# Kernel optimization log

Measured on AMD Instinct MI355X. Metric: run time of the kernel, lower is better.

## Reference

```python
import jax, jax.numpy as jnp
import numpy as np

N_PRED = 10000
N_GT = 1000
NUM_CLASSES = 80
IMG_H = 800
IMG_W = 1333
EPS = 1e-12
ALPHA, GAMMA, CLS_W = 0.25, 2.0, 2.0
L1_W, IOU_W = 5.0, 2.0
CENTER_RADIUS = 2.5
CAND_TOPK = 5


def _make_boxes(key, n, w, h):
    k1, k2 = jax.random.split(key)
    cxcy = jax.random.uniform(k1, (n, 2)) * jnp.array([w, h], jnp.float32)
    wh = jax.random.uniform(k2, (n, 2)) * 190.0 + 10.0
    return jnp.concatenate([cxcy - wh / 2, cxcy + wh / 2], axis=1).astype(jnp.float32)


def setup_inputs() -> dict:
    key = jax.random.key(0)
    k1, k2, k3, k4 = jax.random.split(key, 4)
    return {
        'pred_logits': jax.random.normal(k1, (N_PRED, NUM_CLASSES), jnp.float32),
        'pred_boxes': _make_boxes(k2, N_PRED, IMG_W, IMG_H),
        'gt_bboxes': _make_boxes(k3, N_GT, IMG_W, IMG_H),
        'gt_labels': jax.random.randint(k4, (N_GT,), 0, NUM_CLASSES),
        'img_h': IMG_H,
        'img_w': IMG_W,
    }


def _pairwise_iou_giou(pred, gt):
    area_p = (pred[:, 2] - pred[:, 0]) * (pred[:, 3] - pred[:, 1])
    area_g = (gt[:, 2] - gt[:, 0]) * (gt[:, 3] - gt[:, 1])
    lt = jnp.maximum(pred[:, None, :2], gt[None, :, :2])
    rb = jnp.minimum(pred[:, None, 2:], gt[None, :, 2:])
    wh = jnp.clip(rb - lt, 0.0)
    inter = wh[..., 0] * wh[..., 1]                       # [N,G]
    union = area_p[:, None] + area_g[None, :] - inter
    iou = inter / jnp.maximum(union, EPS)
    elt = jnp.minimum(pred[:, None, :2], gt[None, :, :2])
    erb = jnp.maximum(pred[:, None, 2:], gt[None, :, 2:])
    ewh = jnp.clip(erb - elt, 0.0)
    enclose = ewh[..., 0] * ewh[..., 1]
    giou = iou - (enclose - union) / jnp.maximum(enclose, EPS)
    return iou, giou


def _center_info(pred, gt):
    # pred/gt in xyxy; uses pred box centers, strict inequalities as in source
    pcx = (pred[:, 0] + pred[:, 2]) * 0.5
    pcy = (pred[:, 1] + pred[:, 3]) * 0.5
    gx1, gy1, gx2, gy2 = gt[:, 0], gt[:, 1], gt[:, 2], gt[:, 3]
    in_boxes = ((pcx[:, None] > gx1) & (pcx[:, None] < gx2) &
                (pcy[:, None] > gy1) & (pcy[:, None] < gy2))
    gcx, gcy = (gx1 + gx2) * 0.5, (gy1 + gy2) * 0.5
    gw, gh = gx2 - gx1, gy2 - gy1
    r = CENTER_RADIUS
    in_centers = ((pcx[:, None] > gcx - r * gw) & (pcx[:, None] < gcx + r * gw) &
                  (pcy[:, None] > gcy - r * gh) & (pcy[:, None] < gcy + r * gh))
    valid = in_boxes.any(1) | in_centers.any(1)
    return valid, in_boxes & in_centers


def _compute_cost_and_ious(pred_logits, pred_boxes, gt_bboxes, gt_labels, img_h, img_w):
    # FocalLossCost
    p = jax.nn.sigmoid(pred_logits)
    neg = -jnp.log1p(-(p - EPS)) * (1 - ALPHA) * p ** GAMMA
    pos = -jnp.log(p + EPS) * ALPHA * (1 - p) ** GAMMA
    cls_cost = (pos - neg)[:, gt_labels] * CLS_W            # [N,G]
    # BBoxL1Cost (normalized by image size)
    factor = jnp.array([img_w, img_h, img_w, img_h], jnp.float32)
    l1_cost = jnp.sum(jnp.abs(pred_boxes[:, None, :] / factor -
                              gt_bboxes[None, :, :] / factor), -1) * L1_W
    # IoUCost (giou) + pairwise ious for dynamic-k
    ious, giou = _pairwise_iou_giou(pred_boxes, gt_bboxes)
    iou_cost = -giou * IOU_W
    valid_mask, in_boxes_and_center = _center_info(pred_boxes, gt_bboxes)
    cost = cls_cost + l1_cost + iou_cost + jnp.where(in_boxes_and_center, 0.0, 100.0)
    cost = cost + jnp.where(valid_mask, 0.0, 10000.0)[:, None]
    return cost, ious


def _dynamic_k_matching(cost, ious):
    n, g = cost.shape
    k = min(CAND_TOPK, n)
    topk_ious, _ = jax.lax.top_k(ious.T, k)                 # [G,k]
    dynamic_ks = jnp.maximum(topk_ious.sum(1).astype(jnp.int32), 1)
    _, idx = jax.lax.top_k(-cost.T, k)                      # [G,k] smallest costs per gt
    vals = (jnp.arange(k)[None, :] < dynamic_ks[:, None]).astype(cost.dtype)
    cols = jnp.broadcast_to(jnp.arange(g)[:, None], (g, k))
    mm = jnp.zeros_like(cost).at[idx, cols].max(vals)       # scatter 1s per gt column
    # resolve priors matched to >1 gt (note: mask is reused stale inside the loop, as in source)
    prior_mask = mm.sum(1) > 1
    cmin = jnp.argmin(cost, axis=1)
    mm = jnp.where(prior_mask[:, None], jax.nn.one_hot(cmin, g, dtype=cost.dtype), mm)

    def cond(state):
        m, _ = state
        return jnp.any(m.sum(0) == 0)

    def body(state):
        m, c = state
        matched_q = m.sum(1) > 0
        c = c + 100000.0 * matched_q[:, None].astype(c.dtype)
        unmatched = m.sum(0) == 0
        pos = jnp.argmin(c, axis=0)                         # [G]
        oh = jax.nn.one_hot(pos, n, dtype=c.dtype).T        # [N,G]
        m = jnp.where(unmatched[None, :], oh, m)
        cmin2 = jnp.argmin(c, axis=1)
        m_fix = jnp.where(prior_mask[:, None], jax.nn.one_hot(cmin2, g, dtype=c.dtype), m)
        m = jnp.where(jnp.any(m.sum(1) > 1), m_fix, m)
        return (m, c)

    mm, _ = jax.lax.while_loop(cond, body, (mm, cost))
    fg_mask = mm.sum(1) > 0
    matched = jnp.argmax(mm, axis=1).astype(jnp.int32)
    return fg_mask, jnp.where(fg_mask, matched, 0)


def reference(pred_logits, pred_boxes, gt_bboxes, gt_labels, img_h, img_w):
    cost, ious = _compute_cost_and_ious(pred_logits, pred_boxes, gt_bboxes,
                                        gt_labels, img_h, img_w)
    fg_mask, matched_gt = _dynamic_k_matching(cost, ious)
    # dense form: matched_gt[i] valid only where fg_mask[i] (fixed-shape version of
    # the original's compressed matched_gt_inds = mm[fg_mask].argmax(1))
    return fg_mask, matched_gt
```

## Files before the change

### kernel.cpp

```cpp
#include <hip/hip_runtime.h>
#include <cfloat>
#include <cmath>

#define NP 10000
#define NG 1000
#define NC 80
#define LMAX 6
#define NCH 4
#define CHSZ (NP / NCH)
#define WMAIN 39
#define WTAIL 4

#define S_MULTI 12
#define S_BODY  16
#define RI_BIG  0x3fffffff
#define KMAX    0xFFFFFFFFFFFFFFFFull

#define TKEY    0xC248000000000000ull

#define WCAP    768

__device__ __forceinline__ bool lexless(float av, int ai, float bv, int bi) {
    return (av < bv) || (av == bv && ai < bi);
}

__device__ __forceinline__ unsigned long long packkey(float v, int idx) {
    unsigned u = __float_as_uint(v);
    u ^= (unsigned)(((int)u) >> 31) | 0x80000000u;
    return ((unsigned long long)u << 32) | (unsigned)idx;
}
__device__ __forceinline__ int keyidx(unsigned long long k) {
    return (int)(unsigned)(k & 0xFFFFFFFFu);
}

__device__ __forceinline__ float inflate(float c, int k) {
    for (int q = 0; q < k; q++) c += 100000.0f;
    return c;
}

__device__ __forceinline__ void cost_iou(float4 p, float4 pn, float4 pi,
        float4 g, float4 cb, float4 Gn, float ga, float clsv,
        float& cc_out, float& iou_out) {
#pragma clang fp contract(off)
    float wx = fminf(p.z, g.z) - fmaxf(p.x, g.x); wx = fmaxf(wx, 0.0f);
    float wy = fminf(p.w, g.w) - fmaxf(p.y, g.y); wy = fmaxf(wy, 0.0f);
    float inter = wx * wy;
    float uni = pi.z + ga - inter;
    float iou = inter / fmaxf(uni, 1e-12f);
    float ex = fmaxf(p.z, g.z) - fminf(p.x, g.x); ex = fmaxf(ex, 0.0f);
    float ey = fmaxf(p.w, g.w) - fminf(p.y, g.y); ey = fmaxf(ey, 0.0f);
    float enc = ex * ey;
    float giou = iou - (enc - uni) / fmaxf(enc, 1e-12f);
    float l1 = ((fabsf(pn.x - Gn.x) + fabsf(pn.y - Gn.y))
                + fabsf(pn.z - Gn.z)) + fabsf(pn.w - Gn.w);
    float cc = clsv + l1 * 5.0f;
    cc = cc + (-giou * 2.0f);
    bool inb = (pi.x > g.x && pi.x < g.z && pi.y > g.y && pi.y < g.w);
    bool inc = (pi.x > cb.x && pi.x < cb.z && pi.y > cb.y && pi.y < cb.w);
    cc = cc + ((inb && inc) ? 0.0f : 100.0f);
    cc = cc + pi.w;
    cc_out = cc; iou_out = iou;
}

__device__ __forceinline__ void ins5k(unsigned long long* kv,
        unsigned long long key) {
    if (key < kv[4]) {
        kv[4] = key;
#pragma unroll
        for (int t = 4; t > 0; t--)
            if (kv[t] < kv[t-1]) { unsigned long long tv = kv[t]; kv[t] = kv[t-1]; kv[t-1] = tv; }
    }
}
__device__ __forceinline__ void ins5i(float* iv, float iou) {
    if (iou > iv[4]) {
        iv[4] = iou;
#pragma unroll
        for (int t = 4; t > 0; t--)
            if (iv[t] > iv[t-1]) { float tv = iv[t]; iv[t] = iv[t-1]; iv[t-1] = tv; }
    }
}

__device__ __forceinline__ void cswapk(unsigned long long& a,
        unsigned long long& b) {
    unsigned long long lo = (a < b) ? a : b;
    unsigned long long hi = (a < b) ? b : a;
    a = lo; b = hi;
}
__device__ __forceinline__ void sort5k(unsigned long long* a) {
    cswapk(a[0],a[1]); cswapk(a[3],a[4]); cswapk(a[2],a[4]);
    cswapk(a[2],a[3]); cswapk(a[1],a[4]); cswapk(a[0],a[3]);
    cswapk(a[0],a[2]); cswapk(a[1],a[3]); cswapk(a[1],a[2]);
}
__device__ __forceinline__ void cswapi(float& a, float& b) {
    float hi = fmaxf(a, b), lo = fminf(a, b);
    a = hi; b = lo;
}
__device__ __forceinline__ void sort5i(float* a) {
    cswapi(a[0],a[1]); cswapi(a[3],a[4]); cswapi(a[2],a[4]);
    cswapi(a[2],a[3]); cswapi(a[1],a[4]); cswapi(a[0],a[3]);
    cswapi(a[0],a[2]); cswapi(a[1],a[3]); cswapi(a[1],a[2]);
}

__device__ __forceinline__ void wavemerge5(unsigned long long* kv, float* iv) {
#pragma unroll
    for (int d = 1; d < 64; d <<= 1) {
        unsigned long long r0 = __shfl_xor(kv[0], d);
        unsigned long long r1 = __shfl_xor(kv[1], d);
        unsigned long long r2 = __shfl_xor(kv[2], d);
        unsigned long long r3 = __shfl_xor(kv[3], d);
        unsigned long long r4 = __shfl_xor(kv[4], d);
        kv[0] = (kv[0] < r4) ? kv[0] : r4;
        kv[1] = (kv[1] < r3) ? kv[1] : r3;
        kv[2] = (kv[2] < r2) ? kv[2] : r2;
        kv[3] = (kv[3] < r1) ? kv[3] : r1;
        kv[4] = (kv[4] < r0) ? kv[4] : r0;
        sort5k(kv);
        float s0 = __shfl_xor(iv[0], d);
        float s1 = __shfl_xor(iv[1], d);
        float s2 = __shfl_xor(iv[2], d);
        float s3 = __shfl_xor(iv[3], d);
        float s4 = __shfl_xor(iv[4], d);
        iv[0] = fmaxf(iv[0], s4);
        iv[1] = fmaxf(iv[1], s3);
        iv[2] = fmaxf(iv[2], s2);
        iv[3] = fmaxf(iv[3], s1);
        iv[4] = fmaxf(iv[4], s0);
        sort5i(iv);
    }
}

#define CLS_TI 64
#define PB_CLS0 40
#define PB_G0   197
#define PB_V0   201
__global__ __launch_bounds__(256) void k_prep(const float* __restrict__ logits,
        const float* __restrict__ pb, const float* __restrict__ gb,
        const int* __restrict__ imgw, const int* __restrict__ imgh,
        float* __restrict__ clsval, float4* __restrict__ pnorm,
        float4* __restrict__ pinfo, float4* __restrict__ gcb,
        float4* __restrict__ gnm, float* __restrict__ gar,
        int* rowcnt, int* rowfirst, int* rowiter, int* prior, int* priorcol,
        int* colsum, int* scal)
{
    __shared__ float sl[CLS_TI * (NC + 1)];
    int b = blockIdx.x;
    if (b < PB_CLS0) {
        int i = b * 256 + threadIdx.x;
        if (i < NP) {
            rowcnt[i] = 0; rowfirst[i] = 0x7fffffff; rowiter[i] = RI_BIG;
            prior[i] = 0; priorcol[i] = 0;
        }
        if (i < NG) colsum[i] = 0;
        if (i < 32) scal[i] = 0;
    } else if (b < PB_G0) {
        int i0 = (b - PB_CLS0) * CLS_TI;
        bool full = (i0 + CLS_TI) <= NP;
        if (full) {
            const float* src = logits + (size_t)i0 * NC;
            for (int e = threadIdx.x; e < CLS_TI * NC; e += 256) {
                int di = e / NC, c = e - di * NC;
                sl[di * (NC + 1) + c] = src[e];
            }
        } else {
            for (int e = threadIdx.x; e < CLS_TI * NC; e += 256) {
                int di = e / NC, c = e - di * NC;
                int i = i0 + di;
                sl[di * (NC + 1) + c] = (i < NP) ? logits[(size_t)i * NC + c] : 0.0f;
            }
        }
        __syncthreads();
        for (int e = threadIdx.x; e < CLS_TI * NC; e += 256) {
            int c = e >> 6, di = e & 63;
            int i = i0 + di;
            if (i >= NP) continue;
            float x = sl[di * (NC + 1) + c];
            float p = 1.0f / (1.0f + expf(-x));
            float neg = -log1pf(-(p - 1e-12f)) * 0.75f * (p * p);
            float om = 1.0f - p;
            float pos = -logf(p + 1e-12f) * 0.25f * (om * om);
            clsval[(size_t)c * NP + i] = (pos - neg) * 2.0f;
        }
    } else if (b < PB_V0) {
#pragma clang fp contract(off)
        int j = (b - PB_G0) * 256 + threadIdx.x;
        if (j < NG) {
            float fw = (float)imgw[0], fh = (float)imgh[0];
            float4 g = ((const float4*)gb)[j];
            float gcx = (g.x + g.z) * 0.5f, gcy = (g.y + g.w) * 0.5f;
            float gw = g.z - g.x, gh = g.w - g.y;
            float4 cb; cb.x = gcx - 2.5f * gw; cb.y = gcy - 2.5f * gh;
            cb.z = gcx + 2.5f * gw; cb.w = gcy + 2.5f * gh;
            gcb[j] = cb;
            float4 Gn; Gn.x = g.x / fw; Gn.y = g.y / fh; Gn.z = g.z / fw; Gn.w = g.w / fh;
            gnm[j] = Gn;
            gar[j] = (g.z - g.x) * (g.w - g.y);
        }
    } else {
#pragma clang fp contract(off)
        int wave = threadIdx.x >> 6;
        int lane = threadIdx.x & 63;
        int i = (b - PB_V0) * 4 + wave;
        if (i >= NP) return;
        float4 p = ((const float4*)pb)[i];
        float pcx = (p.x + p.z) * 0.5f, pcy = (p.y + p.w) * 0.5f;
        int vb = 0, vc = 0;
        const float4* gb4 = (const float4*)gb;
        for (int jb = 0; jb < NG; jb += 64) {
            int j = jb + lane;
            if (j < NG) {
                float4 g = gb4[j];
                vb |= (pcx > g.x && pcx < g.z && pcy > g.y && pcy < g.w) ? 1 : 0;
                float gcx = (g.x + g.z) * 0.5f, gcy = (g.y + g.w) * 0.5f;
                float gw = g.z - g.x, gh = g.w - g.y;
                vc |= (pcx > gcx - 2.5f * gw && pcx < gcx + 2.5f * gw &&
                       pcy > gcy - 2.5f * gh && pcy < gcy + 2.5f * gh) ? 1 : 0;
            }
            if (__any(vb | vc)) break;
        }
        int any = __any(vb | vc) ? 1 : 0;
        if (lane == 0) {
            float fw = (float)imgw[0], fh = (float)imgh[0];
            float4 pn; pn.x = p.x / fw; pn.y = p.y / fh; pn.z = p.z / fw; pn.w = p.w / fh;
            pnorm[i] = pn;
            float4 pi4; pi4.x = pcx; pi4.y = pcy;
            pi4.z = (p.z - p.x) * (p.w - p.y);
            pi4.w = any ? 0.0f : 10000.0f;
            pinfo[i] = pi4;
        }
    }
}

__global__ __launch_bounds__(256) void k_cost2(
        const float* __restrict__ pb, const float* __restrict__ gb,
        const int* __restrict__ glab, const float* __restrict__ clsval,
        const float4* __restrict__ pnorm, const float4* __restrict__ pinfo,
        const float4* __restrict__ gcb, const float4* __restrict__ gnm,
        const float* __restrict__ gar,
        int* __restrict__ rowcnt, int* __restrict__ rowfirst,
        int* __restrict__ rowiter, int* __restrict__ top5,
        int* __restrict__ dkarr)
{
    __shared__ int s_list[4 * WCAP];
    __shared__ unsigned long long s_k4[4][5];
    __shared__ float s_iv4[4][5];
    __shared__ int s_redo;

    int j = blockIdx.x;
    int tid = threadIdx.x;
    int wid = tid >> 6;
    int ln  = tid & 63;
    float4 g  = ((const float4*)gb)[j];
    float4 cb = gcb[j];
    float4 Gn = gnm[j];
    float  ga = gar[j];
    const float* clscol = clsval + (size_t)glab[j] * NP;
    const float4* pb4 = (const float4*)pb;
    int base_i = wid * CHSZ;

    int wbase = 0;
    for (int k = 0; k <= WMAIN; k++) {
        bool valid = (k < WMAIN) | (ln < WTAIL);
        int i = base_i + ln + k * 64;
        float4 p = pb4[valid ? i : base_i];
        bool o = valid & (p.z > g.x) & (g.z > p.x) & (p.w > g.y) & (g.w > p.y);
        unsigned long long m = __ballot(o ? 1 : 0);
        if (o) {
            int slot = wbase + __popcll(m & ((1ull << ln) - 1ull));
            if (slot < WCAP) s_list[wid * WCAP + slot] = i;
        }
        wbase += __popcll(m);
    }
    int cnt = wbase;
    bool overflow = (cnt > WCAP);

    unsigned long long kv[5]; float iv[5];
#pragma unroll
    for (int t = 0; t < 5; t++) { kv[t] = KMAX; iv[t] = overflow ? -1.0f : 0.0f; }

    if (!overflow) {
        for (int q = ln; q < cnt; q += 64) {
            int i = s_list[wid * WCAP + q];
            float cc, iou;
            cost_iou(pb4[i], pnorm[i], pinfo[i], g, cb, Gn, ga, clscol[i], cc, iou);
            ins5k(kv, packkey(cc, i)); ins5i(iv, iou);
        }
    } else {
        for (int k = 0; k <= WMAIN; k++) {
            bool valid = (k < WMAIN) | (ln < WTAIL);
            if (valid) {
                int i = base_i + ln + k * 64;
                float cc, iou;
                cost_iou(pb4[i], pnorm[i], pinfo[i], g, cb, Gn, ga, clscol[i], cc, iou);
                ins5k(kv, packkey(cc, i)); ins5i(iv, iou);
            }
        }
    }
    wavemerge5(kv, iv);

    if (ln == 0) {
#pragma unroll
        for (int t = 0; t < 5; t++) { s_k4[wid][t] = kv[t]; s_iv4[wid][t] = iv[t]; }
    }
    __syncthreads();

    unsigned long long mk0=KMAX, mk1=KMAX, mk2=KMAX, mk3=KMAX, mk4=KMAX;
    float mi0=-2.0f, mi1=-2.0f, mi2=-2.0f, mi3=-2.0f, mi4=-2.0f;
    if (tid == 0) {
        int h0 = 0, h1 = 0, h2 = 0, h3 = 0;
        unsigned long long mk[5];
#pragma unroll
        for (int r = 0; r < 5; r++) {
            unsigned long long v0 = (h0 < 5) ? s_k4[0][h0] : KMAX;
            unsigned long long v1 = (h1 < 5) ? s_k4[1][h1] : KMAX;
            unsigned long long v2 = (h2 < 5) ? s_k4[2][h2] : KMAX;
            unsigned long long v3 = (h3 < 5) ? s_k4[3][h3] : KMAX;
            unsigned long long best = v0; int sel = 0;
            if (v1 < best) { best = v1; sel = 1; }
            if (v2 < best) { best = v2; sel = 2; }
            if (v3 < best) { best = v3; sel = 3; }
            mk[r] = best;
            h0 += (sel == 0); h1 += (sel == 1); h2 += (sel == 2); h3 += (sel == 3);
        }
        int g0 = 0, g1 = 0, g2 = 0, g3 = 0;
        float mi[5];
#pragma unroll
        for (int r = 0; r < 5; r++) {
            float w0 = (g0 < 5) ? s_iv4[0][g0] : -2.0f;
            float w1 = (g1 < 5) ? s_iv4[1][g1] : -2.0f;
            float w2 = (g2 < 5) ? s_iv4[2][g2] : -2.0f;
            float w3 = (g3 < 5) ? s_iv4[3][g3] : -2.0f;
            float best = w0; int sel = 0;
            if (w1 > best) { best = w1; sel = 1; }
            if (w2 > best) { best = w2; sel = 2; }
            if (w3 > best) { best = w3; sel = 3; }
            mi[r] = best;
            g0 += (sel == 0); g1 += (sel == 1); g2 += (sel == 2); g3 += (sel == 3);
        }
        mk0 = mk[0]; mk1 = mk[1]; mk2 = mk[2]; mk3 = mk[3]; mk4 = mk[4];
        mi0 = mi[0]; mi1 = mi[1]; mi2 = mi[2]; mi3 = mi[3]; mi4 = mi[4];
        s_redo = (mk4 >= TKEY) ? 1 : 0;
    }
    __syncthreads();

    if (s_redo) {
#pragma unroll
        for (int t = 0; t < 5; t++) { kv[t] = KMAX; iv[t] = -1.0f; }
        for (int k = 0; k <= WMAIN; k++) {
            bool valid = (k < WMAIN) | (ln < WTAIL);
            if (valid) {
                int i = base_i + ln + k * 64;
                float cc, iou;
                cost_iou(pb4[i], pnorm[i], pinfo[i], g, cb, Gn, ga, clscol[i], cc, iou);
                ins5k(kv, packkey(cc, i)); ins5i(iv, iou);
            }
        }
        wavemerge5(kv, iv);
        if (ln == 0) {
#pragma unroll
            for (int t = 0; t < 5; t++) { s_k4[wid][t] = kv[t]; s_iv4[wid][t] = iv[t]; }
        }
        __syncthreads();
        if (tid == 0) {
            int h0 = 0, h1 = 0, h2 = 0, h3 = 0;
            unsigned long long mk[5];
#pragma unroll
            for (int r = 0; r < 5; r++) {
                unsigned long long v0 = (h0 < 5) ? s_k4[0][h0] : KMAX;
                unsigned long long v1 = (h1 < 5) ? s_k4[1][h1] : KMAX;
                unsigned long long v2 = (h2 < 5) ? s_k4[2][h2] : KMAX;
                unsigned long long v3 = (h3 < 5) ? s_k4[3][h3] : KMAX;
                unsigned long long best = v0; int sel = 0;
                if (v1 < best) { best = v1; sel = 1; }
                if (v2 < best) { best = v2; sel = 2; }
                if (v3 < best) { best = v3; sel = 3; }
                mk[r] = best;
                h0 += (sel == 0); h1 += (sel == 1); h2 += (sel == 2); h3 += (sel == 3);
            }
            int g0 = 0, g1 = 0, g2 = 0, g3 = 0;
            float mi[5];
#pragma unroll
            for (int r = 0; r < 5; r++) {
                float w0 = (g0 < 5) ? s_iv4[0][g0] : -2.0f;
                float w1 = (g1 < 5) ? s_iv4[1][g1] : -2.0f;
                float w2 = (g2 < 5) ? s_iv4[2][g2] : -2.0f;
                float w3 = (g3 < 5) ? s_iv4[3][g3] : -2.0f;
                float best = w0; int sel = 0;
                if (w1 > best) { best = w1; sel = 1; }
                if (w2 > best) { best = w2; sel = 2; }
                if (w3 > best) { best = w3; sel = 3; }
                mi[r] = best;
                g0 += (sel == 0); g1 += (sel == 1); g2 += (sel == 2); g3 += (sel == 3);
            }
            mk0 = mk[0]; mk1 = mk[1]; mk2 = mk[2]; mk3 = mk[3]; mk4 = mk[4];
            mi0 = mi[0]; mi1 = mi[1]; mi2 = mi[2]; mi3 = mi[3]; mi4 = mi[4];
        }
    }

    if (tid == 0) {
        float s = (((mi0 + mi1) + mi2) + mi3) + mi4;
        int dk = (int)s;
        if (dk < 1) dk = 1;
        dkarr[j] = dk;
        int b0 = keyidx(mk0), b1 = keyidx(mk1), b2 = keyidx(mk2);
        int b3 = keyidx(mk3), b4 = keyidx(mk4);
        top5[j * 5 + 0] = b0; top5[j * 5 + 1] = b1; top5[j * 5 + 2] = b2;
        top5[j * 5 + 3] = b3; top5[j * 5 + 4] = b4;
        int bs0 = b0, bs1 = b1, bs2 = b2, bs3 = b3, bs4 = b4;
#pragma unroll
        for (int t = 0; t < 5; t++) {
            int r = (t == 0) ? bs0 : (t == 1) ? bs1 : (t == 2) ? bs2
                  : (t == 3) ? bs3 : bs4;
            if (t < dk) {
                atomicAdd(&rowcnt[r], 1);
                atomicMin(&rowfirst[r], j);
                atomicMin(&rowiter[r], -1);
            }
        }
    }
}

__global__ __launch_bounds__(256) void k_pfixsurv(const float* __restrict__ pb,
        const float* __restrict__ gb, const int* __restrict__ glab,
        const float* __restrict__ clsval,
        const float4* __restrict__ pnorm, const float4* __restrict__ pinfo,
        const float4* __restrict__ gcb, const float4* __restrict__ gnm,
        const float* __restrict__ gar,
        int* __restrict__ prior, int* __restrict__ priorcol,
        int* __restrict__ colsum,
        const int* __restrict__ rowcnt, const int* __restrict__ top5,
        const int* __restrict__ dkarr)
{
    int b = blockIdx.x;
    int tid = threadIdx.x;
    if (b >= 2500) {
        int j = (b - 2500) * 256 + tid;
        if (j >= NG) return;
        int c = 0;
        int dk = dkarr[j];
        for (int t = 0; t < dk; t++) if (rowcnt[top5[j * 5 + t]] == 1) c++;
        if (c) atomicAdd(&colsum[j], c);
        return;
    }
    __shared__ float rv[256]; __shared__ int ri[256];
    for (int q = 0; q < 4; q++) {
        int row = b * 4 + q;
        if (rowcnt[row] <= 1) continue;
        if (tid == 0) prior[row] = 1;
        float4 p = ((const float4*)pb)[row];
        float4 pn = pnorm[row];
        float4 pi4 = pinfo[row];
        float best = FLT_MAX; int bj = 0x7fffffff;
        for (int j = tid; j < NG; j += 256) {
            float cc, iou;
            cost_iou(p, pn, pi4, ((const float4*)gb)[j], gcb[j], gnm[j], gar[j],
                     clsval[(size_t)glab[j] * NP + row], cc, iou);
            if (lexless(cc, j, best, bj)) { best = cc; bj = j; }
        }
        rv[tid] = best; ri[tid] = bj; __syncthreads();
        for (int w = 128; w > 0; w >>= 1) {
            if (tid < w) {
                float ov = rv[tid + w]; int oi = ri[tid + w];
                if (lexless(ov, oi, rv[tid], ri[tid])) { rv[tid] = ov; ri[tid] = oi; }
            }
            __syncthreads();
        }
        if (tid == 0) {
            priorcol[row] = ri[0];
            atomicAdd(&colsum[ri[0]], 1);
        }
        __syncthreads();
    }
}

__global__ __launch_bounds__(256) void k_iterB(const float* __restrict__ pb,
        const float* __restrict__ gb, const int* __restrict__ glab,
        const float* __restrict__ clsval,
        const float4* __restrict__ pnorm, const float4* __restrict__ pinfo,
        const float4* __restrict__ gcb, const float4* __restrict__ gnm,
        const float* __restrict__ gar, const int* __restrict__ top5,
        int* __restrict__ rowiter, int* __restrict__ rowcnt,
        int* __restrict__ rowfirst, int* __restrict__ colsum,
        int* __restrict__ scal, int t)
{
    int j = blockIdx.x;
    if (colsum[j] != 0) return;
    int tid = threadIdx.x;
    if (tid == 0) scal[S_BODY + t] = 1;

    __shared__ int s_pos;
    if (tid == 0) {
        int pos = -1;
        for (int r = 0; r < 5; r++) {
            int i = top5[j * 5 + r];
            if (rowiter[i] >= t) { pos = i; break; }
        }
        s_pos = pos;
    }
    __syncthreads();
    int pos = s_pos;

    if (pos < 0) {
        float4 g  = ((const float4*)gb)[j];
        float4 cb = gcb[j];
        float4 Gn = gnm[j];
        float  ga = gar[j];
        const float* clscol = clsval + (size_t)glab[j] * NP;
        const float4* pb4 = (const float4*)pb;
        __shared__ float rv[256]; __shared__ int ri[256];
        float best = FLT_MAX; int bi = 0x7fffffff;
        for (int i = tid; i < NP; i += 256) {
            if (rowiter[i] < t) continue;
            float cc, iou;
            cost_iou(pb4[i], pnorm[i], pinfo[i], g, cb, Gn, ga, clscol[i], cc, iou);
            if (lexless(cc, i, best, bi)) { best = cc; bi = i; }
        }
        rv[tid] = best; ri[tid] = bi; __syncthreads();
        for (int w = 128; w > 0; w >>= 1) {
            if (tid < w) {
                float ov = rv[tid + w]; int oi = ri[tid + w];
                if (lexless(ov, oi, rv[tid], ri[tid])) { rv[tid] = ov; ri[tid] = oi; }
            }
            __syncthreads();
        }
        pos = ri[0];
    }

    if (tid == 0) {
        colsum[j] = 1;
        int old = atomicAdd(&rowcnt[pos], 1);
        if (old >= 1) scal[S_MULTI] = 1;
        atomicMin(&rowfirst[pos], j);
        atomicMin(&rowiter[pos], t);
    }
}

__global__ __launch_bounds__(256) void k_iterC(const float* __restrict__ pb,
        const float* __restrict__ gb, const int* __restrict__ glab,
        const float* __restrict__ clsval,
        const float4* __restrict__ pnorm, const float4* __restrict__ pinfo,
        const float4* __restrict__ gcb, const float4* __restrict__ gnm,
        const float* __restrict__ gar,
        const int* __restrict__ prior, const int* __restrict__ rowiter,
        int* __restrict__ priorcol, int* __restrict__ colsum,
        int* __restrict__ scal, int t)
{
    if (scal[S_BODY + t] == 0 || scal[S_MULTI] == 0) return;
    int b = blockIdx.x;
    int tid = threadIdx.x;
    __shared__ float rv[256]; __shared__ int ri[256];
    for (int q = 0; q < 4; q++) {
        int row = b * 4 + q;
        if (!prior[row]) continue;
        int k = t - rowiter[row]; if (k < 0) k = 0;
        float4 p = ((const float4*)pb)[row];
        float4 pn = pnorm[row];
        float4 pi4 = pinfo[row];
        float best = FLT_MAX; int bj = 0x7fffffff;
        for (int j = tid; j < NG; j += 256) {
            float cc, iou;
            cost_iou(p, pn, pi4, ((const float4*)gb)[j], gcb[j], gnm[j], gar[j],
                     clsval[(size_t)glab[j] * NP + row], cc, iou);
            float val = inflate(cc, k);
            if (lexless(val, j, best, bj)) { best = val; bj = j; }
        }
        rv[tid] = best; ri[tid] = bj; __syncthreads();
        for (int w = 128; w > 0; w >>= 1) {
            if (tid < w) {
                float ov = rv[tid + w]; int oi = ri[tid + w];
                if (lexless(ov, oi, rv[tid], ri[tid])) { rv[tid] = ov; ri[tid] = oi; }
            }
            __syncthreads();
        }
        if (tid == 0) {
            int nb = ri[0];
            int oldc = priorcol[row];
            if (nb != oldc) {
                atomicSub(&colsum[oldc], 1);
                atomicAdd(&colsum[nb], 1);
                priorcol[row] = nb;
            }
        }
        __syncthreads();
    }
}

__global__ __launch_bounds__(256) void k_final(const int* __restrict__ rowcnt,
        const int* __restrict__ prior, const int* __restrict__ priorcol,
        const int* __restrict__ rowfirst, int* __restrict__ out)
{
    int i = blockIdx.x * 256 + threadIdx.x;
    if (i >= NP) return;
    int fg = rowcnt[i] > 0;
    out[i] = fg ? 1 : 0;
    out[NP + i] = fg ? (prior[i] ? priorcol[i] : rowfirst[i]) : 0;
}

extern "C" void kernel_launch(void* const* d_in, const int* in_sizes, int n_in,
                              void* d_out, int out_size, void* d_ws, size_t ws_size,
                              hipStream_t stream)
{
    (void)in_sizes; (void)n_in; (void)out_size; (void)ws_size;
    const float* logits = (const float*)d_in[0];
    const float* pboxes = (const float*)d_in[1];
    const float* gboxes = (const float*)d_in[2];
    const int*   glab   = (const int*)d_in[3];
    const int*   imgh   = (const int*)d_in[4];
    const int*   imgw   = (const int*)d_in[5];
    int* out = (int*)d_out;

    char* w = (char*)d_ws;
    float*  clsval  = (float*)(w);
    float4* pnorm   = (float4*)(w + 3200000);
    float4* pinfo   = (float4*)(w + 3360000);
    float4* gcb     = (float4*)(w + 3520000);
    float4* gnm     = (float4*)(w + 3536000);
    float*  gar     = (float*)(w + 3552000);
    int* rowcnt     = (int*)(w + 3556000);
    int* rowfirst   = (int*)(w + 3596000);
    int* rowiter    = (int*)(w + 3636000);
    int* prior      = (int*)(w + 3676000);
    int* priorcol   = (int*)(w + 3716000);
    int* top5       = (int*)(w + 3756000);
    int* dkarr      = (int*)(w + 3776000);
    int* colsum     = (int*)(w + 3780000);
    int* scal       = (int*)(w + 3784000);

    hipLaunchKernelGGL(k_prep, dim3(2701), dim3(256), 0, stream,
                       logits, pboxes, gboxes, imgw, imgh,
                       clsval, pnorm, pinfo, gcb, gnm, gar,
                       rowcnt, rowfirst, rowiter, prior, priorcol, colsum, scal);
    hipLaunchKernelGGL(k_cost2, dim3(NG), dim3(256), 0, stream,
                       pboxes, gboxes, glab, clsval, pnorm, pinfo, gcb, gnm, gar,
                       rowcnt, rowfirst, rowiter, top5, dkarr);
    hipLaunchKernelGGL(k_pfixsurv, dim3(2504), dim3(256), 0, stream,
                       pboxes, gboxes, glab, clsval, pnorm, pinfo, gcb, gnm, gar,
                       prior, priorcol, colsum, rowcnt, top5, dkarr);
    for (int t = 0; t < LMAX; t++) {
        hipLaunchKernelGGL(k_iterB, dim3(NG), dim3(256), 0, stream,
                           pboxes, gboxes, glab, clsval, pnorm, pinfo, gcb, gnm, gar,
                           top5, rowiter, rowcnt, rowfirst, colsum, scal, t);
        hipLaunchKernelGGL(k_iterC, dim3(2500), dim3(256), 0, stream,
                           pboxes, gboxes, glab, clsval, pnorm, pinfo, gcb, gnm, gar,
                           prior, rowiter, priorcol, colsum, scal, t);
    }
    hipLaunchKernelGGL(k_final, dim3(40), dim3(256), 0, stream,
                       rowcnt, prior, priorcol, rowfirst, out);
}
```

Before: 155.0 us.

## Fuse iterative matching loop into single-block persistent kernel with cached prior-row costs

Replaces the 12 per-iteration launches of k_iterB/k_iterC plus k_final with one single-block 1024-thread kernel that runs all iterations internally, using shared-memory lists of prior rows and of columns needing a full scan. k_pfixsurv now caches the cost rows of multi-matched priors in a workspace buffer, so later iterations re-read costs instead of recomputing them. Wave-level shuffle reductions replace the shared-memory tree reductions. This removes launch overhead and redundant cost evaluation, but the whole dynamic phase runs on a single CU, so any fallback full scans over 10000 predictions become much slower.

```diff
diff --git a/kernel.cpp b/kernel.cpp
--- a/kernel.cpp
+++ b/kernel.cpp
@@ -11,14 +11,16 @@
 #define WMAIN 39
 #define WTAIL 4
 
-#define S_MULTI 12
-#define S_BODY  16
 #define RI_BIG  0x3fffffff
 #define KMAX    0xFFFFFFFFFFFFFFFFull
 
 #define TKEY    0xC248000000000000ull
 
 #define WCAP    768
+
+#define PSLOTS  2560
+#define PCAP    2560
+#define FCAP    1024
 
 __device__ __forceinline__ bool lexless(float av, int ai, float bv, int bi) {
     return (av < bv) || (av == bv && ai < bi);
@@ -129,6 +131,15 @@
     }
 }
 
+__device__ __forceinline__ void wavered_lex(float& best, int& bi) {
+#pragma unroll
+    for (int d = 1; d < 64; d <<= 1) {
+        float ov = __shfl_xor(best, d);
+        int oi = __shfl_xor(bi, d);
+        if (lexless(ov, oi, best, bi)) { best = ov; bi = oi; }
+    }
+}
+
 #define CLS_TI 64
 #define PB_CLS0 40
 #define PB_G0   197
@@ -140,7 +151,7 @@
         float4* __restrict__ pinfo, float4* __restrict__ gcb,
         float4* __restrict__ gnm, float* __restrict__ gar,
         int* rowcnt, int* rowfirst, int* rowiter, int* prior, int* priorcol,
-        int* colsum, int* scal)
+        int* colsum, int* scal, int* priorslot)
 {
     __shared__ float sl[CLS_TI * (NC + 1)];
     int b = blockIdx.x;
@@ -148,7 +159,7 @@
         int i = b * 256 + threadIdx.x;
         if (i < NP) {
             rowcnt[i] = 0; rowfirst[i] = 0x7fffffff; rowiter[i] = RI_BIG;
-            prior[i] = 0; priorcol[i] = 0;
+            prior[i] = 0; priorcol[i] = 0; priorslot[i] = -1;
         }
         if (i < NG) colsum[i] = 0;
         if (i < 32) scal[i] = 0;
@@ -405,11 +416,10 @@
         int b3 = keyidx(mk3), b4 = keyidx(mk4);
         top5[j * 5 + 0] = b0; top5[j * 5 + 1] = b1; top5[j * 5 + 2] = b2;
         top5[j * 5 + 3] = b3; top5[j * 5 + 4] = b4;
-        int bs0 = b0, bs1 = b1, bs2 = b2, bs3 = b3, bs4 = b4;
 #pragma unroll
         for (int t = 0; t < 5; t++) {
-            int r = (t == 0) ? bs0 : (t == 1) ? bs1 : (t == 2) ? bs2
-                  : (t == 3) ? bs3 : bs4;
+            int r = (t == 0) ? b0 : (t == 1) ? b1 : (t == 2) ? b2
+                  : (t == 3) ? b3 : b4;
             if (t < dk) {
                 atomicAdd(&rowcnt[r], 1);
                 atomicMin(&rowfirst[r], j);
@@ -428,7 +438,9 @@
         int* __restrict__ prior, int* __restrict__ priorcol,
         int* __restrict__ colsum,
         const int* __restrict__ rowcnt, const int* __restrict__ top5,
-        const int* __restrict__ dkarr)
+        const int* __restrict__ dkarr,
+        int* __restrict__ scal, int* __restrict__ priorslot,
+        float* __restrict__ rowcost)
 {
     int b = blockIdx.x;
     int tid = threadIdx.x;
@@ -442,10 +454,20 @@
         return;
     }
     __shared__ float rv[256]; __shared__ int ri[256];
+    __shared__ int s_slot;
     for (int q = 0; q < 4; q++) {
         int row = b * 4 + q;
         if (rowcnt[row] <= 1) continue;
-        if (tid == 0) prior[row] = 1;
+        if (tid == 0) {
+            prior[row] = 1;
+            int s = atomicAdd(&scal[20], 1);
+            int sl = (s < PSLOTS) ? s : -1;
+            priorslot[row] = sl;
+            s_slot = sl;
+        }
+        __syncthreads();
+        int slot = s_slot;
+        float* rc = (slot >= 0) ? (rowcost + (size_t)slot * NG) : nullptr;
         float4 p = ((const float4*)pb)[row];
         float4 pn = pnorm[row];
         float4 pi4 = pinfo[row];
@@ -454,6 +476,7 @@
             float cc, iou;
             cost_iou(p, pn, pi4, ((const float4*)gb)[j], gcb[j], gnm[j], gar[j],
                      clsval[(size_t)glab[j] * NP + row], cc, iou);
+            if (rc) rc[j] = cc;
             if (lexless(cc, j, best, bj)) { best = cc; bj = j; }
         }
         rv[tid] = best; ri[tid] = bj; __syncthreads();
@@ -472,127 +495,145 @@
     }
 }
 
-__global__ __launch_bounds__(256) void k_iterB(const float* __restrict__ pb,
-        const float* __restrict__ gb, const int* __restrict__ glab,
-        const float* __restrict__ clsval,
-        const float4* __restrict__ pnorm, const float4* __restrict__ pinfo,
-        const float4* __restrict__ gcb, const float4* __restrict__ gnm,
-        const float* __restrict__ gar, const int* __restrict__ top5,
-        int* __restrict__ rowiter, int* __restrict__ rowcnt,
-        int* __restrict__ rowfirst, int* __restrict__ colsum,
-        int* __restrict__ scal, int t)
-{
-    int j = blockIdx.x;
-    if (colsum[j] != 0) return;
-    int tid = threadIdx.x;
-    if (tid == 0) scal[S_BODY + t] = 1;
-
-    __shared__ int s_pos;
-    if (tid == 0) {
-        int pos = -1;
-        for (int r = 0; r < 5; r++) {
-            int i = top5[j * 5 + r];
-            if (rowiter[i] >= t) { pos = i; break; }
-        }
-        s_pos = pos;
-    }
-    __syncthreads();
-    int pos = s_pos;
-
-    if (pos < 0) {
-        float4 g  = ((const float4*)gb)[j];
-        float4 cb = gcb[j];
-        float4 Gn = gnm[j];
-        float  ga = gar[j];
-        const float* clscol = clsval + (size_t)glab[j] * NP;
-        const float4* pb4 = (const float4*)pb;
-        __shared__ float rv[256]; __shared__ int ri[256];
-        float best = FLT_MAX; int bi = 0x7fffffff;
-        for (int i = tid; i < NP; i += 256) {
-            if (rowiter[i] < t) continue;
-            float cc, iou;
-            cost_iou(pb4[i], pnorm[i], pinfo[i], g, cb, Gn, ga, clscol[i], cc, iou);
-            if (lexless(cc, i, best, bi)) { best = cc; bi = i; }
-        }
-        rv[tid] = best; ri[tid] = bi; __syncthreads();
-        for (int w = 128; w > 0; w >>= 1) {
-            if (tid < w) {
-                float ov = rv[tid + w]; int oi = ri[tid + w];
-                if (lexless(ov, oi, rv[tid], ri[tid])) { rv[tid] = ov; ri[tid] = oi; }
-            }
-            __syncthreads();
-        }
-        pos = ri[0];
-    }
-
-    if (tid == 0) {
-        colsum[j] = 1;
-        int old = atomicAdd(&rowcnt[pos], 1);
-        if (old >= 1) scal[S_MULTI] = 1;
-        atomicMin(&rowfirst[pos], j);
-        atomicMin(&rowiter[pos], t);
-    }
-}
-
-__global__ __launch_bounds__(256) void k_iterC(const float* __restrict__ pb,
-        const float* __restrict__ gb, const int* __restrict__ glab,
-        const float* __restrict__ clsval,
+__global__ __launch_bounds__(1024) void k_dyn(
+        const float* __restrict__ pb, const float* __restrict__ gb,
+        const int* __restrict__ glab, const float* __restrict__ clsval,
         const float4* __restrict__ pnorm, const float4* __restrict__ pinfo,
         const float4* __restrict__ gcb, const float4* __restrict__ gnm,
         const float* __restrict__ gar,
-        const int* __restrict__ prior, const int* __restrict__ rowiter,
-        int* __restrict__ priorcol, int* __restrict__ colsum,
-        int* __restrict__ scal, int t)
+        const int* __restrict__ top5, int* __restrict__ rowiter,
+        int* __restrict__ rowcnt, int* __restrict__ rowfirst,
+        int* __restrict__ colsum, const int* __restrict__ prior,
+        int* __restrict__ priorcol, const int* __restrict__ priorslot,
+        const float* __restrict__ rowcost, int* __restrict__ out)
 {
-    if (scal[S_BODY + t] == 0 || scal[S_MULTI] == 0) return;
-    int b = blockIdx.x;
+    __shared__ int s_plist[PCAP];
+    __shared__ int s_flist[FCAP];
+    __shared__ int s_pcnt;
+    __shared__ int s_fcnt;
+    __shared__ int s_body;
+    __shared__ int s_multi;
+
     int tid = threadIdx.x;
-    __shared__ float rv[256]; __shared__ int ri[256];
-    for (int q = 0; q < 4; q++) {
-        int row = b * 4 + q;
-        if (!prior[row]) continue;
-        int k = t - rowiter[row]; if (k < 0) k = 0;
-        float4 p = ((const float4*)pb)[row];
-        float4 pn = pnorm[row];
-        float4 pi4 = pinfo[row];
-        float best = FLT_MAX; int bj = 0x7fffffff;
-        for (int j = tid; j < NG; j += 256) {
-            float cc, iou;
-            cost_iou(p, pn, pi4, ((const float4*)gb)[j], gcb[j], gnm[j], gar[j],
-                     clsval[(size_t)glab[j] * NP + row], cc, iou);
-            float val = inflate(cc, k);
-            if (lexless(val, j, best, bj)) { best = val; bj = j; }
-        }
-        rv[tid] = best; ri[tid] = bj; __syncthreads();
-        for (int w = 128; w > 0; w >>= 1) {
-            if (tid < w) {
-                float ov = rv[tid + w]; int oi = ri[tid + w];
-                if (lexless(ov, oi, rv[tid], ri[tid])) { rv[tid] = ov; ri[tid] = oi; }
-            }
-            __syncthreads();
-        }
-        if (tid == 0) {
-            int nb = ri[0];
-            int oldc = priorcol[row];
-            if (nb != oldc) {
-                atomicSub(&colsum[oldc], 1);
-                atomicAdd(&colsum[nb], 1);
-                priorcol[row] = nb;
-            }
-        }
-        __syncthreads();
-    }
-}
-
-__global__ __launch_bounds__(256) void k_final(const int* __restrict__ rowcnt,
-        const int* __restrict__ prior, const int* __restrict__ priorcol,
-        const int* __restrict__ rowfirst, int* __restrict__ out)
-{
-    int i = blockIdx.x * 256 + threadIdx.x;
-    if (i >= NP) return;
-    int fg = rowcnt[i] > 0;
-    out[i] = fg ? 1 : 0;
-    out[NP + i] = fg ? (prior[i] ? priorcol[i] : rowfirst[i]) : 0;
+    int wid = tid >> 6;
+    int ln  = tid & 63;
+    const float4* pb4 = (const float4*)pb;
+
+    if (tid == 0) { s_pcnt = 0; s_multi = 0; }
+    __syncthreads();
+    for (int i = tid; i < NP; i += 1024) {
+        if (prior[i]) {
+            int s = atomicAdd(&s_pcnt, 1);
+            if (s < PCAP) s_plist[s] = i;
+        }
+    }
+    __syncthreads();
+    int pcnt = (s_pcnt < PCAP) ? s_pcnt : PCAP;
+
+    for (int t = 0; t < LMAX; t++) {
+        if (tid == 0) { s_body = 0; s_fcnt = 0; }
+        __threadfence();
+        __syncthreads();
+
+        for (int j = tid; j < NG; j += 1024) {
+            if (colsum[j] != 0) continue;
+            s_body = 1;
+            int pos = -1;
+            for (int r = 0; r < 5; r++) {
+                int i = top5[j * 5 + r];
+                if (rowiter[i] >= t) { pos = i; break; }
+            }
+            if (pos < 0) {
+                int f = atomicAdd(&s_fcnt, 1);
+                if (f < FCAP) s_flist[f] = j;
+                continue;
+            }
+            colsum[j] = 1;
+            int old = atomicAdd(&rowcnt[pos], 1);
+            if (old >= 1) s_multi = 1;
+            atomicMin(&rowfirst[pos], j);
+            atomicMin(&rowiter[pos], t);
+        }
+        __threadfence();
+        __syncthreads();
+
+        int fcnt = (s_fcnt < FCAP) ? s_fcnt : FCAP;
+        for (int q = wid; q < fcnt; q += 16) {
+            int j = s_flist[q];
+            float4 g  = ((const float4*)gb)[j];
+            float4 cb = gcb[j];
+            float4 Gn = gnm[j];
+            float  ga = gar[j];
+            const float* clscol = clsval + (size_t)glab[j] * NP;
+            float best = FLT_MAX; int bi = 0x7fffffff;
+            for (int i = ln; i < NP; i += 64) {
+                if (rowiter[i] < t) continue;
+                float cc, iou;
+                cost_iou(pb4[i], pnorm[i], pinfo[i], g, cb, Gn, ga, clscol[i], cc, iou);
+                if (lexless(cc, i, best, bi)) { best = cc; bi = i; }
+            }
+            wavered_lex(best, bi);
+            if (ln == 0) {
+                colsum[j] = 1;
+                int old = atomicAdd(&rowcnt[bi], 1);
+                if (old >= 1) s_multi = 1;
+                atomicMin(&rowfirst[bi], j);
+                atomicMin(&rowiter[bi], t);
+            }
+        }
+        __threadfence();
+        __syncthreads();
+
+        if (!s_body) break;
+
+        if (s_multi) {
+            for (int q = wid; q < pcnt; q += 16) {
+                int row = s_plist[q];
+                int k = t - rowiter[row]; if (k < 0) k = 0;
+                int slot = priorslot[row];
+                float best = FLT_MAX; int bj = 0x7fffffff;
+                if (slot >= 0) {
+                    const float* rc = rowcost + (size_t)slot * NG;
+                    for (int j = ln; j < NG; j += 64) {
+                        float val = inflate(rc[j], k);
+                        if (lexless(val, j, best, bj)) { best = val; bj = j; }
+                    }
+                } else {
+                    float4 p = pb4[row];
+                    float4 pn = pnorm[row];
+                    float4 pi4 = pinfo[row];
+                    for (int j = ln; j < NG; j += 64) {
+                        float cc, iou;
+                        cost_iou(p, pn, pi4, ((const float4*)gb)[j], gcb[j],
+                                 gnm[j], gar[j],
+                                 clsval[(size_t)glab[j] * NP + row], cc, iou);
+                        float val = inflate(cc, k);
+                        if (lexless(val, j, best, bj)) { best = val; bj = j; }
+                    }
+                }
+                wavered_lex(best, bj);
+                if (ln == 0) {
+                    int nb = bj;
+                    int oldc = priorcol[row];
+                    if (nb != oldc) {
+                        atomicSub(&colsum[oldc], 1);
+                        atomicAdd(&colsum[nb], 1);
+                        priorcol[row] = nb;
+                    }
+                }
+            }
+        }
+        __threadfence();
+        __syncthreads();
+    }
+
+    __threadfence();
+    __syncthreads();
+    for (int i = tid; i < NP; i += 1024) {
+        int fg = rowcnt[i] > 0;
+        out[i] = fg ? 1 : 0;
+        out[NP + i] = fg ? (prior[i] ? priorcol[i] : rowfirst[i]) : 0;
+    }
 }
 
 extern "C" void kernel_launch(void* const* d_in, const int* in_sizes, int n_in,
@@ -624,25 +665,23 @@
     int* dkarr      = (int*)(w + 3776000);
     int* colsum     = (int*)(w + 3780000);
     int* scal       = (int*)(w + 3784000);
+    int* priorslot  = (int*)(w + 3784128);
+    float* rowcost  = (float*)(w + 3824128);
 
     hipLaunchKernelGGL(k_prep, dim3(2701), dim3(256), 0, stream,
                        logits, pboxes, gboxes, imgw, imgh,
                        clsval, pnorm, pinfo, gcb, gnm, gar,
-                       rowcnt, rowfirst, rowiter, prior, priorcol, colsum, scal);
+                       rowcnt, rowfirst, rowiter, prior, priorcol, colsum, scal,
+                       priorslot);
     hipLaunchKernelGGL(k_cost2, dim3(NG), dim3(256), 0, stream,
                        pboxes, gboxes, glab, clsval, pnorm, pinfo, gcb, gnm, gar,
                        rowcnt, rowfirst, rowiter, top5, dkarr);
     hipLaunchKernelGGL(k_pfixsurv, dim3(2504), dim3(256), 0, stream,
                        pboxes, gboxes, glab, clsval, pnorm, pinfo, gcb, gnm, gar,
-                       prior, priorcol, colsum, rowcnt, top5, dkarr);
-    for (int t = 0; t < LMAX; t++) {
-        hipLaunchKernelGGL(k_iterB, dim3(NG), dim3(256), 0, stream,
-                           pboxes, gboxes, glab, clsval, pnorm, pinfo, gcb, gnm, gar,
-                           top5, rowiter, rowcnt, rowfirst, colsum, scal, t);
-        hipLaunchKernelGGL(k_iterC, dim3(2500), dim3(256), 0, stream,
-                           pboxes, gboxes, glab, clsval, pnorm, pinfo, gcb, gnm, gar,
-                           prior, rowiter, priorcol, colsum, scal, t);
-    }
-    hipLaunchKernelGGL(k_final, dim3(40), dim3(256), 0, stream,
-                       rowcnt, prior, priorcol, rowfirst, out);
-}
+                       prior, priorcol, colsum, rowcnt, top5, dkarr,
+                       scal, priorslot, rowcost);
+    hipLaunchKernelGGL(k_dyn, dim3(1), dim3(1024), 0, stream,
+                       pboxes, gboxes, glab, clsval, pnorm, pinfo, gcb, gnm, gar,
+                       top5, rowiter, rowcnt, rowfirst, colsum, prior,
+                       priorcol, priorslot, rowcost, out);
+}
```

New measurement: 175.3 us. +13.1%, slower.
